# Kernel optimization log

Hardware: AMD Instinct MI355X
Metric: run time of the kernel (lower is better)

Reference implementation:

```python
import math
import jax, jax.numpy as jnp
import numpy as np

D_MODEL = 1024
D_CTX = 1024
NUM_HEADS = 16
ATTN_DIM = 1024
HEAD_DIM = ATTN_DIM // NUM_HEADS  # 64
ROPE_GAMMA = 10.0
ROTARY_BASE = 10000.0
ATTN_SCALE = math.sqrt(ATTN_DIM)  # note: module scales by sqrt(attn_dim), not sqrt(head_dim)


def _apply_rope(x, cos, sin):
    # x: [H,B,T,D]; cos/sin: [1,B,T,D//2]
    half = x.shape[-1] // 2
    x1, x2 = x[..., :half], x[..., half:]
    return jnp.concatenate([x1 * cos - x2 * sin, x1 * sin + x2 * cos], axis=-1)


def setup_inputs() -> dict:
    key = jax.random.key(0)
    ks = jax.random.split(key, 12)
    B, T, L = 4, 1024, 1024
    x = jax.random.normal(ks[0], (B, D_MODEL, T), jnp.float32)
    context = jax.random.normal(ks[1], (B, L, D_CTX), jnp.float32)
    # prefix (padding) masks with per-example valid lengths, as in real padded batches
    lens_q = jnp.array([1024, 896, 768, 640])
    lens_k = jnp.array([1024, 960, 832, 704])
    x_mask = (jnp.arange(T)[None, :] < lens_q[:, None]).astype(jnp.int32)[:, None, :]  # [B,1,T]
    context_mask = (jnp.arange(L)[None, :] < lens_k[:, None]).astype(jnp.int32)[:, None, :]  # [B,1,L]
    s = 0.02
    Wq = jax.random.normal(ks[2], (D_MODEL, ATTN_DIM), jnp.float32) * s
    bq = jax.random.normal(ks[3], (ATTN_DIM,), jnp.float32) * s
    Wk = jax.random.normal(ks[4], (D_CTX, ATTN_DIM), jnp.float32) * s
    bk = jax.random.normal(ks[5], (ATTN_DIM,), jnp.float32) * s
    Wv = jax.random.normal(ks[6], (D_CTX, ATTN_DIM), jnp.float32) * s
    bv = jax.random.normal(ks[7], (ATTN_DIM,), jnp.float32) * s
    Wo = jax.random.normal(ks[8], (ATTN_DIM, D_MODEL), jnp.float32) * s
    bo = jax.random.normal(ks[9], (D_MODEL,), jnp.float32) * s
    return {"x": x, "context": context, "x_mask": x_mask, "context_mask": context_mask,
            "Wq": Wq, "bq": bq, "Wk": Wk, "bk": bk, "Wv": Wv, "bv": bv, "Wo": Wo, "bo": bo}


def reference(x, context, x_mask, context_mask, Wq, bq, Wk, bk, Wv, bv, Wo, bo):
    B, _, T = x.shape
    L = context.shape[1]
    H, D = NUM_HEADS, HEAD_DIM
    xm = x_mask.astype(jnp.float32)          # [B,1,T]
    cmf = context_mask.astype(jnp.float32)   # [B,1,L]

    q = jnp.swapaxes(x, 1, 2) @ Wq + bq      # [B,T,attn_dim]
    k = context @ Wk + bk                    # [B,L,attn_dim]
    v = context @ Wv + bv                    # [B,L,attn_dim]

    q = q.reshape(B, T, H, D).transpose(2, 0, 1, 3)  # [H,B,T,D]
    k = k.reshape(B, L, H, D).transpose(2, 0, 1, 3)  # [H,B,L,D]
    v = v.reshape(B, L, H, D).transpose(2, 0, 1, 3)  # [H,B,L,D]

    # length-normalized RoPE (LARoPE)
    len_q = xm.sum(axis=(-2, -1)).reshape(-1, 1, 1)   # [B,1,1]
    len_k = cmf.sum(axis=(-2, -1)).reshape(-1, 1, 1)  # [B,1,1]
    pos_q = jnp.arange(T, dtype=jnp.float32).reshape(1, -1, 1)
    pos_k = jnp.arange(L, dtype=jnp.float32).reshape(1, -1, 1)
    inv_freq = 1.0 / (ROTARY_BASE ** (jnp.arange(0, D, 2, dtype=jnp.float32) / D))
    theta = (inv_freq * ROPE_GAMMA).reshape(1, 1, -1)  # [1,1,D//2]
    freqs_q = (pos_q / len_q) * theta  # [B,T,D//2]
    freqs_k = (pos_k / len_k) * theta  # [B,L,D//2]
    q = _apply_rope(q, jnp.cos(freqs_q)[None], jnp.sin(freqs_q)[None])
    k = _apply_rope(k, jnp.cos(freqs_k)[None], jnp.sin(freqs_k)[None])

    logits = jnp.einsum('hbtd,hbld->hbtl', q, k) / ATTN_SCALE  # [H,B,T,L]
    key_pad = (context_mask == 0)[None]  # [1,B,1,L]
    logits = jnp.where(key_pad, -jnp.inf, logits)
    attn = jax.nn.softmax(logits, axis=-1)
    query_pad = (x_mask == 0).transpose(1, 0, 2)[..., None]  # [1,B,T,1]
    attn = jnp.where(query_pad, 0.0, attn)

    out = jnp.einsum('hbtl,hbld->hbtd', attn, v)          # [H,B,T,D]
    out = out.transpose(1, 2, 0, 3).reshape(B, T, ATTN_DIM)
    out = out @ Wo + bo                                   # [B,T,d_model]
    out = out * jnp.swapaxes(xm, 1, 2)                    # [B,T,1] broadcast
    return jnp.swapaxes(out, 1, 2)                        # [B,d_model,T]
```

## Files before the change

kernel.cpp:

```cpp
#include <hip/hip_runtime.h>
#include <hip/hip_bf16.h>

typedef __attribute__((ext_vector_type(8))) short s8v;
typedef __attribute__((ext_vector_type(4))) float f4v;
typedef __attribute__((ext_vector_type(4))) unsigned short u4v;
typedef __attribute__((ext_vector_type(2))) unsigned int u2v;

#define NH 16

__device__ __forceinline__ unsigned short f2bf(float f) {
  union { float f; unsigned int u; } v; v.f = f;
  unsigned int r = (v.u + 0x7fffu + ((v.u >> 16) & 1u)) >> 16;
  return (unsigned short)r;
}
__device__ __forceinline__ void gll16(const void* g, void* l) {
  __builtin_amdgcn_global_load_lds((const __attribute__((address_space(1))) void*)g,
                                   (__attribute__((address_space(3))) void*)l, 16, 0, 0);
}
__device__ __forceinline__ unsigned int cvtpk(float lo, float hi) {
  unsigned int r;
  asm volatile("v_cvt_pk_bf16_f32 %0, %1, %2" : "=v"(r) : "v"(lo), "v"(hi));
  return r;
}

__global__ __launch_bounds__(256) void prep_kernel(
    const float* __restrict__ x, const float* __restrict__ ctx,
    const float* __restrict__ Wq, const float* __restrict__ Wk,
    const float* __restrict__ Wv, const float* __restrict__ Wo,
    const int* __restrict__ xm, const int* __restrict__ cm,
    unsigned short* __restrict__ xT, unsigned short* __restrict__ ctxb,
    unsigned short* __restrict__ WqT, unsigned short* __restrict__ WkT,
    unsigned short* __restrict__ WvT, unsigned short* __restrict__ WoT,
    float* __restrict__ lens) {
  const int z = blockIdx.z;
  const int tid = threadIdx.x;
  if (z == 12) {
    if (blockIdx.x | blockIdx.y) return;
    const int w = tid >> 6, lane = tid & 63;
    const int g = w * 2 + (lane >> 5);
    const int l32 = lane & 31;
    const int* m = (g < 4) ? (xm + g * 1024) : (cm + (g - 4) * 1024);
    int s = 0;
    for (int i = l32; i < 1024; i += 32) s += m[i];
    for (int o = 16; o; o >>= 1) s += __shfl_xor(s, o);
    if (l32 == 0) lens[g] = (float)s;
    return;
  }
  if (z >= 8) {
    const float* in = ctx + ((size_t)(z - 8) << 20);
    unsigned short* out = ctxb + ((size_t)(z - 8) << 20);
    const int i = (blockIdx.y * 32 + blockIdx.x) * 1024 + tid * 4;
    const f4v v = *(const f4v*)&in[i];
    u4v o;
#pragma unroll
    for (int j = 0; j < 4; ++j) o[j] = f2bf(v[j]);
    *(u4v*)&out[i] = o;
    return;
  }
  __shared__ unsigned short tile[32][33];
  const float* in;
  unsigned short* out;
  if (z < 4)      { in = x + ((size_t)z << 20); out = xT + ((size_t)z << 20); }
  else if (z == 4){ in = Wq; out = WqT; }
  else if (z == 5){ in = Wk; out = WkT; }
  else if (z == 6){ in = Wv; out = WvT; }
  else            { in = Wo; out = WoT; }
  const int r0 = blockIdx.y * 32, c0 = blockIdx.x * 32;
  const int tx = tid & 31, ty = tid >> 5;
  for (int i = ty; i < 32; i += 8) tile[i][tx] = f2bf(in[(size_t)(r0 + i) * 1024 + c0 + tx]);
  __syncthreads();
  for (int i = ty; i < 32; i += 8) out[(size_t)(c0 + i) * 1024 + r0 + tx] = tile[tx][i];
}

__global__ __launch_bounds__(256) void gemm_qkv_kernel(
    const unsigned short* __restrict__ xT, const unsigned short* __restrict__ ctxb,
    const unsigned short* __restrict__ WqT, const unsigned short* __restrict__ WkT,
    const unsigned short* __restrict__ WvT,
    const float* __restrict__ bq, const float* __restrict__ bk, const float* __restrict__ bv,
    unsigned short* __restrict__ Qb, unsigned short* __restrict__ Kb,
    unsigned short* __restrict__ Vtb, const float* __restrict__ lens) {
  __shared__ __attribute__((aligned(16))) unsigned short As[8192];
  __shared__ __attribute__((aligned(16))) unsigned short Bs[8192];
  const int mode = blockIdx.z;
  const unsigned short* A  = (mode == 0) ? xT : ctxb;
  const unsigned short* Bt = (mode == 0) ? WqT : (mode == 1) ? WkT : WvT;
  const float* bias        = (mode == 0) ? bq : (mode == 1) ? bk : bv;
  const int tid = threadIdx.x;
  const int lane = tid & 63, w = tid >> 6;
  const int lq = lane & 15, lg = lane >> 4;
  const int m0 = blockIdx.y * 128, n0 = blockIdx.x * 128;
  const int wm = (w & 1) * 64, wn = (w >> 1) * 64;
  const int cswz = (lq & 7) << 3;
  f4v acc[4][4] = {};

  for (int kt = 0; kt < 16; ++kt) {
    const int k0 = kt * 64;
#pragma unroll
    for (int i = 0; i < 4; ++i) {
      const int ci = i * 256 + tid;
      const int row = ci >> 3;
      const int col = ((ci & 7) * 8) ^ ((row & 7) << 3);
      gll16(&A[(size_t)(m0 + row) * 1024 + k0 + col], &As[ci * 8]);
      gll16(&Bt[(size_t)(n0 + row) * 1024 + k0 + col], &Bs[ci * 8]);
    }
    __syncthreads();
#pragma unroll
    for (int kc = 0; kc < 2; ++kc) {
      s8v af[4], bfr[4];
#pragma unroll
      for (int i = 0; i < 4; ++i)
        af[i] = *(const s8v*)&As[(wm + i * 16 + lq) * 64 + ((kc * 32 + lg * 8) ^ cswz)];
#pragma unroll
      for (int i = 0; i < 4; ++i)
        bfr[i] = *(const s8v*)&Bs[(wn + i * 16 + lq) * 64 + ((kc * 32 + lg * 8) ^ cswz)];
#pragma unroll
      for (int mi = 0; mi < 4; ++mi)
#pragma unroll
        for (int ni = 0; ni < 4; ++ni)
          acc[mi][ni] = __builtin_amdgcn_mfma_f32_16x16x32_bf16(af[mi], bfr[ni], acc[mi][ni], 0, 0, 0);
    }
    __syncthreads();
  }

  float bv4[4];
#pragma unroll
  for (int ni = 0; ni < 4; ++ni) bv4[ni] = bias[n0 + wn + ni * 16 + lq];
  const int b = m0 >> 10;

  if (mode <= 1) {
    unsigned short* O = mode ? Kb : Qb;
    const float len = lens[(mode ? 4 : 0) + b];
    const int h = (n0 + wn) >> 6;
#pragma unroll
    for (int mi = 0; mi < 4; ++mi) {
#pragma unroll
      for (int rr = 0; rr < 4; ++rr) {
        const int m = m0 + wm + mi * 16 + lg * 4 + rr;
        const int t = m & 1023;
        const float fb = (float)t / len * 10.0f;
#pragma unroll
        for (int ni = 0; ni < 2; ++ni) {
          const int jj = ni * 16 + lq;
          const float freq = fb * __expf((float)jj * -0.28782313662425572f);
          float sn, cs;
          __sincosf(freq, &sn, &cs);
          const float x1 = acc[mi][ni][rr] + bv4[ni];
          const float x2 = acc[mi][ni + 2][rr] + bv4[ni + 2];
          unsigned short* bp = &O[((size_t)((b * NH + h) * 1024 + t)) * 64 + jj];
          bp[0] = f2bf(x1 * cs - x2 * sn);
          bp[32] = f2bf(x1 * sn + x2 * cs);
        }
      }
    }
  } else {
#pragma unroll
    for (int mi = 0; mi < 4; ++mi) {
      const int mbase = m0 + wm + mi * 16 + lg * 4;
      const int l0 = mbase & 1023;
#pragma unroll
      for (int ni = 0; ni < 4; ++ni) {
        const int n = n0 + wn + ni * 16 + lq;
        const int hh = n >> 6, d = n & 63;
        u4v pk;
#pragma unroll
        for (int rr = 0; rr < 4; ++rr) pk[rr] = f2bf(acc[mi][ni][rr] + bv4[ni]);
        *(u4v*)&Vtb[((size_t)((b * NH + hh) * 64 + d)) * 1024 + l0] = pk;
      }
    }
  }
}

__global__ __launch_bounds__(256) void gemm_o_kernel(
    const unsigned short* __restrict__ A, const unsigned short* __restrict__ Bt,
    const float* __restrict__ bias, float* __restrict__ Cout,
    const int* __restrict__ xmask) {
  __shared__ __attribute__((aligned(16))) unsigned short As[8192];
  __shared__ __attribute__((aligned(16))) unsigned short Bs[8192];
  const int tid = threadIdx.x;
  const int lane = tid & 63, w = tid >> 6;
  const int lq = lane & 15, lg = lane >> 4;
  const int m0 = blockIdx.y * 128, n0 = blockIdx.x * 128;
  const int wm = (w & 1) * 64, wn = (w >> 1) * 64;
  const int cswz = (lq & 7) << 3;
  f4v acc[4][4] = {};

  for (int kt = 0; kt < 16; ++kt) {
    const int k0 = kt * 64;
#pragma unroll
    for (int i = 0; i < 4; ++i) {
      const int ci = i * 256 + tid;
      const int row = ci >> 3;
      const int col = ((ci & 7) * 8) ^ ((row & 7) << 3);
      gll16(&A[(size_t)(m0 + row) * 1024 + k0 + col], &As[ci * 8]);
      gll16(&Bt[(size_t)(n0 + row) * 1024 + k0 + col], &Bs[ci * 8]);
    }
    __syncthreads();
#pragma unroll
    for (int kc = 0; kc < 2; ++kc) {
      s8v af[4], bfr[4];
#pragma unroll
      for (int i = 0; i < 4; ++i)
        af[i] = *(const s8v*)&As[(wm + i * 16 + lq) * 64 + ((kc * 32 + lg * 8) ^ cswz)];
#pragma unroll
      for (int i = 0; i < 4; ++i)
        bfr[i] = *(const s8v*)&Bs[(wn + i * 16 + lq) * 64 + ((kc * 32 + lg * 8) ^ cswz)];
#pragma unroll
      for (int mi = 0; mi < 4; ++mi)
#pragma unroll
        for (int ni = 0; ni < 4; ++ni)
          acc[mi][ni] = __builtin_amdgcn_mfma_f32_16x16x32_bf16(af[mi], bfr[ni], acc[mi][ni], 0, 0, 0);
    }
    __syncthreads();
  }

  float bv4[4];
#pragma unroll
  for (int ni = 0; ni < 4; ++ni) bv4[ni] = bias[n0 + wn + ni * 16 + lq];
  const int b = m0 >> 10;
#pragma unroll
  for (int mi = 0; mi < 4; ++mi) {
    const int mbase = m0 + wm + mi * 16 + lg * 4;
    const int t0 = mbase & 1023;
#pragma unroll
    for (int ni = 0; ni < 4; ++ni) {
      const int n = n0 + wn + ni * 16 + lq;
      f4v pk;
#pragma unroll
      for (int rr = 0; rr < 4; ++rr) {
        float v = acc[mi][ni][rr] + bv4[ni];
        v *= (float)xmask[b * 1024 + t0 + rr];
        pk[rr] = v;
      }
      *(f4v*)&Cout[(size_t)b * 1024 * 1024 + (size_t)n * 1024 + t0] = pk;
    }
  }
}

__global__ __launch_bounds__(512) void attn_kernel(
    const unsigned short* __restrict__ Q, const unsigned short* __restrict__ K,
    const unsigned short* __restrict__ Vt, const float* __restrict__ lens,
    unsigned short* __restrict__ Aout) {
  __shared__ __attribute__((aligned(16))) unsigned short Ks[2][4096];
  __shared__ __attribute__((aligned(16))) unsigned short Vs[2][4096];
  __shared__ __attribute__((aligned(16))) unsigned short Plds[8][16][72];
  const int tid = threadIdx.x;
  const int lane = tid & 63, w = tid >> 6;
  const int lq = lane & 15, lg = lane >> 4;
  const int bh = blockIdx.y;
  const int b = bh >> 4, h = bh & 15;
  const int lenq = (int)lens[b];
  if ((int)blockIdx.x * 128 >= lenq) return;
  const int lenk = (int)lens[4 + b];
  const int nkt = (lenk + 63) >> 6;
  const int qrow = blockIdx.x * 128 + w * 16;
  const unsigned short* Qp = Q + ((size_t)bh * 1024 + qrow) * 64;
  const unsigned short* Kp = K + (size_t)bh * 65536;
  const unsigned short* Vp = Vt + (size_t)bh * 65536;
  const s8v qf0 = *(const s8v*)&Qp[lq * 64 + lg * 8];
  const s8v qf1 = *(const s8v*)&Qp[lq * 64 + 32 + lg * 8];
  const int r0 = tid >> 3;
  const int c0x = ((tid & 7) * 8) ^ ((r0 & 7) << 3);
  const int cswz = (lq & 7) << 3;

  gll16(&Kp[(size_t)r0 * 64 + c0x], &Ks[0][tid * 8]);
  gll16(&Vp[(size_t)r0 * 1024 + c0x], &Vs[0][tid * 8]);
  __syncthreads();

  const float SC2 = 0.0450842200277f;
  float m_run = -1e30f, s_run = 0.0f;
  f4v ot[4] = {};
  for (int kt = 0; kt < nkt; ++kt) {
    const int p = kt & 1;
    if (kt + 1 < nkt) {
      const int kn = (kt + 1) * 64;
      gll16(&Kp[(size_t)(kn + r0) * 64 + c0x], &Ks[p ^ 1][tid * 8]);
      gll16(&Vp[(size_t)r0 * 1024 + kn + c0x], &Vs[p ^ 1][tid * 8]);
    }
    const int k0 = kt * 64;
    const bool full = (k0 + 64 <= lenk);
    float pvv[16];
    float tmax = -1e30f;
    __builtin_amdgcn_s_setprio(1);
#pragma unroll
    for (int kk = 0; kk < 4; ++kk) {
      const int krow = kk * 16 + lq;
      const s8v a0 = *(const s8v*)&Ks[p][krow * 64 + ((lg * 8) ^ cswz)];
      const s8v a1 = *(const s8v*)&Ks[p][krow * 64 + ((32 + lg * 8) ^ cswz)];
      f4v s = {};
      s = __builtin_amdgcn_mfma_f32_16x16x32_bf16(a0, qf0, s, 0, 0, 0);
      s = __builtin_amdgcn_mfma_f32_16x16x32_bf16(a1, qf1, s, 0, 0, 0);
#pragma unroll
      for (int rr = 0; rr < 4; ++rr) {
        float v = s[rr] * SC2;
        if (!full) {
          const int key = k0 + kk * 16 + lg * 4 + rr;
          if (key >= lenk) v = -1e30f;
        }
        pvv[kk * 4 + rr] = v;
        tmax = fmaxf(tmax, v);
      }
    }
    __builtin_amdgcn_s_setprio(0);
    tmax = fmaxf(tmax, __shfl_xor(tmax, 16));
    tmax = fmaxf(tmax, __shfl_xor(tmax, 32));
    if (__any(tmax > m_run + 8.0f)) {
      const float m_new = fmaxf(m_run, tmax);
      const float alpha = exp2f(m_run - m_new);
#pragma unroll
      for (int d = 0; d < 4; ++d)
#pragma unroll
        for (int j = 0; j < 4; ++j) ot[d][j] *= alpha;
      s_run *= alpha;
      m_run = m_new;
    }
    float psum = 0.0f;
#pragma unroll
    for (int kk = 0; kk < 4; ++kk) {
      const float e0 = exp2f(pvv[kk * 4 + 0] - m_run);
      const float e1 = exp2f(pvv[kk * 4 + 1] - m_run);
      const float e2 = exp2f(pvv[kk * 4 + 2] - m_run);
      const float e3 = exp2f(pvv[kk * 4 + 3] - m_run);
      psum += (e0 + e1) + (e2 + e3);
      u2v pw;
      pw[0] = cvtpk(e0, e1);
      pw[1] = cvtpk(e2, e3);
      *(u2v*)&Plds[w][lq][kk * 16 + lg * 4] = pw;
    }
    psum += __shfl_xor(psum, 16);
    psum += __shfl_xor(psum, 32);
    s_run += psum;
    const s8v pb0 = *(const s8v*)&Plds[w][lq][lg * 8];
    const s8v pb1 = *(const s8v*)&Plds[w][lq][32 + lg * 8];
    __builtin_amdgcn_s_setprio(1);
#pragma unroll
    for (int d = 0; d < 4; ++d) {
      const int vrow = d * 16 + lq;
      const s8v av0 = *(const s8v*)&Vs[p][vrow * 64 + ((lg * 8) ^ cswz)];
      const s8v av1 = *(const s8v*)&Vs[p][vrow * 64 + ((32 + lg * 8) ^ cswz)];
      ot[d] = __builtin_amdgcn_mfma_f32_16x16x32_bf16(av0, pb0, ot[d], 0, 0, 0);
      ot[d] = __builtin_amdgcn_mfma_f32_16x16x32_bf16(av1, pb1, ot[d], 0, 0, 0);
    }
    __builtin_amdgcn_s_setprio(0);
    if (kt + 1 < nkt) __syncthreads();
  }
  const float inv = 1.0f / s_run;
  const int t = qrow + lq;
  unsigned short* op = Aout + ((size_t)(b * 1024 + t)) * 1024 + h * 64;
#pragma unroll
  for (int d = 0; d < 4; ++d) {
    u4v oo;
#pragma unroll
    for (int rr = 0; rr < 4; ++rr) oo[rr] = f2bf(ot[d][rr] * inv);
    *(u4v*)&op[d * 16 + lg * 4] = oo;
  }
}

extern "C" void kernel_launch(void* const* d_in, const int* in_sizes, int n_in,
                              void* d_out, int out_size, void* d_ws, size_t ws_size,
                              hipStream_t stream) {
  const float* x   = (const float*)d_in[0];
  const float* ctx = (const float*)d_in[1];
  const int* xm = (const int*)d_in[2];
  const int* cm = (const int*)d_in[3];
  const float* Wq = (const float*)d_in[4];
  const float* bq = (const float*)d_in[5];
  const float* Wk = (const float*)d_in[6];
  const float* bk = (const float*)d_in[7];
  const float* Wv = (const float*)d_in[8];
  const float* bv = (const float*)d_in[9];
  const float* Wo = (const float*)d_in[10];
  const float* bo = (const float*)d_in[11];

  char* ws = (char*)d_ws;
  const size_t MB = 1024 * 1024;
  unsigned short* xT   = (unsigned short*)(ws);
  unsigned short* AOb  = (unsigned short*)(ws);
  unsigned short* ctxb = (unsigned short*)(ws + 8 * MB);
  unsigned short* WqT  = (unsigned short*)(ws + 16 * MB);
  unsigned short* WkT  = (unsigned short*)(ws + 18 * MB);
  unsigned short* WvT  = (unsigned short*)(ws + 20 * MB);
  unsigned short* WoT  = (unsigned short*)(ws + 22 * MB);
  unsigned short* Qb   = (unsigned short*)(ws + 24 * MB);
  unsigned short* Kb   = (unsigned short*)(ws + 32 * MB);
  unsigned short* Vtb  = (unsigned short*)(ws + 40 * MB);
  float* lens          = (float*)(ws + 48 * MB);

  prep_kernel<<<dim3(32, 32, 13), 256, 0, stream>>>(x, ctx, Wq, Wk, Wv, Wo, xm, cm,
                                                    xT, ctxb, WqT, WkT, WvT, WoT, lens);
  gemm_qkv_kernel<<<dim3(8, 32, 3), 256, 0, stream>>>(xT, ctxb, WqT, WkT, WvT,
                                                      bq, bk, bv, Qb, Kb, Vtb, lens);
  attn_kernel<<<dim3(8, 64), 512, 0, stream>>>(Qb, Kb, Vtb, lens, AOb);
  gemm_o_kernel<<<dim3(8, 32), 256, 0, stream>>>(AOb, WoT, bo, (float*)d_out, xm);
}
```

Measured before the change: 125.4 us.

## Precompute RoPE cos/sin table in prep kernel and remap block indices

Adds a prep-kernel slice that recomputes mask lengths and writes a per-batch cos/sin table for Q and K positions, so the QKV GEMM epilogue loads float2 values instead of evaluating exp and sincos per element. It also remaps linear block IDs in the QKV GEMM, output GEMM and attention kernel so neighbouring blocks share M-rows or batch-heads, aiming at better L2 reuse. The cost is a 2 MB table write and read, plus extra blocks in prep, most of which exit immediately.

```diff
diff --git a/kernel.cpp b/kernel.cpp
--- a/kernel.cpp
+++ b/kernel.cpp
@@ -31,7 +31,7 @@
     unsigned short* __restrict__ xT, unsigned short* __restrict__ ctxb,
     unsigned short* __restrict__ WqT, unsigned short* __restrict__ WkT,
     unsigned short* __restrict__ WvT, unsigned short* __restrict__ WoT,
-    float* __restrict__ lens) {
+    float* __restrict__ lens, float2* __restrict__ rope) {
   const int z = blockIdx.z;
   const int tid = threadIdx.x;
   if (z == 12) {
@@ -46,6 +46,30 @@
     if (l32 == 0) lens[g] = (float)s;
     return;
   }
+  if (z == 13) {
+    const int idx = blockIdx.y * 32 + blockIdx.x;
+    if (idx >= 256) return;
+    const int which = idx >> 7;
+    const int b = (idx >> 5) & 3;
+    const int t0 = (idx & 31) * 32;
+    const int* m = (which ? cm : xm) + b * 1024;
+    const int lane = tid & 63;
+    int s = 0;
+    for (int i = lane; i < 1024; i += 64) s += m[i];
+    for (int o = 32; o; o >>= 1) s += __shfl_xor(s, o);
+    const float len = (float)s;
+    const int j = tid & 31;
+    const float theta = 10.0f * __expf((float)j * -0.28782313662425572f);
+    float2* rt = rope + ((size_t)(which * 4 + b) << 15);
+    for (int it = 0; it < 4; ++it) {
+      const int t = t0 + (tid >> 5) + it * 8;
+      const float fr = (float)t / len * theta;
+      float sn, cs;
+      __sincosf(fr, &sn, &cs);
+      rt[t * 32 + j] = make_float2(cs, sn);
+    }
+    return;
+  }
   if (z >= 8) {
     const float* in = ctx + ((size_t)(z - 8) << 20);
     unsigned short* out = ctxb + ((size_t)(z - 8) << 20);
@@ -78,17 +102,21 @@
     const unsigned short* __restrict__ WvT,
     const float* __restrict__ bq, const float* __restrict__ bk, const float* __restrict__ bv,
     unsigned short* __restrict__ Qb, unsigned short* __restrict__ Kb,
-    unsigned short* __restrict__ Vtb, const float* __restrict__ lens) {
+    unsigned short* __restrict__ Vtb, const float2* __restrict__ rope) {
   __shared__ __attribute__((aligned(16))) unsigned short As[8192];
   __shared__ __attribute__((aligned(16))) unsigned short Bs[8192];
-  const int mode = blockIdx.z;
+  const int id = blockIdx.x + (blockIdx.y << 3) + (blockIdx.z << 8);
+  const int rest = id >> 3;
+  const int my = (id & 7) + ((rest & 3) << 3);
+  const int nx = (rest >> 2) & 7;
+  const int mode = rest >> 5;
   const unsigned short* A  = (mode == 0) ? xT : ctxb;
   const unsigned short* Bt = (mode == 0) ? WqT : (mode == 1) ? WkT : WvT;
   const float* bias        = (mode == 0) ? bq : (mode == 1) ? bk : bv;
   const int tid = threadIdx.x;
   const int lane = tid & 63, w = tid >> 6;
   const int lq = lane & 15, lg = lane >> 4;
-  const int m0 = blockIdx.y * 128, n0 = blockIdx.x * 128;
+  const int m0 = my * 128, n0 = nx * 128;
   const int wm = (w & 1) * 64, wn = (w >> 1) * 64;
   const int cswz = (lq & 7) << 3;
   f4v acc[4][4] = {};
@@ -129,7 +157,7 @@
 
   if (mode <= 1) {
     unsigned short* O = mode ? Kb : Qb;
-    const float len = lens[(mode ? 4 : 0) + b];
+    const float2* rt = rope + ((size_t)(mode * 4 + b) << 15);
     const int h = (n0 + wn) >> 6;
 #pragma unroll
     for (int mi = 0; mi < 4; ++mi) {
@@ -137,18 +165,15 @@
       for (int rr = 0; rr < 4; ++rr) {
         const int m = m0 + wm + mi * 16 + lg * 4 + rr;
         const int t = m & 1023;
-        const float fb = (float)t / len * 10.0f;
 #pragma unroll
         for (int ni = 0; ni < 2; ++ni) {
           const int jj = ni * 16 + lq;
-          const float freq = fb * __expf((float)jj * -0.28782313662425572f);
-          float sn, cs;
-          __sincosf(freq, &sn, &cs);
+          const float2 cs2 = rt[t * 32 + jj];
           const float x1 = acc[mi][ni][rr] + bv4[ni];
           const float x2 = acc[mi][ni + 2][rr] + bv4[ni + 2];
           unsigned short* bp = &O[((size_t)((b * NH + h) * 1024 + t)) * 64 + jj];
-          bp[0] = f2bf(x1 * cs - x2 * sn);
-          bp[32] = f2bf(x1 * sn + x2 * cs);
+          bp[0] = f2bf(x1 * cs2.x - x2 * cs2.y);
+          bp[32] = f2bf(x1 * cs2.y + x2 * cs2.x);
         }
       }
     }
@@ -176,10 +201,14 @@
     const int* __restrict__ xmask) {
   __shared__ __attribute__((aligned(16))) unsigned short As[8192];
   __shared__ __attribute__((aligned(16))) unsigned short Bs[8192];
+  const int id = blockIdx.x + (blockIdx.y << 3);
+  const int rest = id >> 3;
+  const int my = (id & 7) + ((rest & 3) << 3);
+  const int nx = rest >> 2;
   const int tid = threadIdx.x;
   const int lane = tid & 63, w = tid >> 6;
   const int lq = lane & 15, lg = lane >> 4;
-  const int m0 = blockIdx.y * 128, n0 = blockIdx.x * 128;
+  const int m0 = my * 128, n0 = nx * 128;
   const int wm = (w & 1) * 64, wn = (w >> 1) * 64;
   const int cswz = (lq & 7) << 3;
   f4v acc[4][4] = {};
@@ -246,13 +275,15 @@
   const int tid = threadIdx.x;
   const int lane = tid & 63, w = tid >> 6;
   const int lq = lane & 15, lg = lane >> 4;
-  const int bh = blockIdx.y;
+  const int id = blockIdx.x + (blockIdx.y << 3);
+  const int bh = (id & 7) + (((id >> 3) & 7) << 3);
+  const int qblk = id >> 6;
   const int b = bh >> 4, h = bh & 15;
   const int lenq = (int)lens[b];
-  if ((int)blockIdx.x * 128 >= lenq) return;
+  if (qblk * 128 >= lenq) return;
   const int lenk = (int)lens[4 + b];
   const int nkt = (lenk + 63) >> 6;
-  const int qrow = blockIdx.x * 128 + w * 16;
+  const int qrow = qblk * 128 + w * 16;
   const unsigned short* Qp = Q + ((size_t)bh * 1024 + qrow) * 64;
   const unsigned short* Kp = K + (size_t)bh * 65536;
   const unsigned short* Vp = Vt + (size_t)bh * 65536;
@@ -384,11 +415,12 @@
   unsigned short* Kb   = (unsigned short*)(ws + 32 * MB);
   unsigned short* Vtb  = (unsigned short*)(ws + 40 * MB);
   float* lens          = (float*)(ws + 48 * MB);
-
-  prep_kernel<<<dim3(32, 32, 13), 256, 0, stream>>>(x, ctx, Wq, Wk, Wv, Wo, xm, cm,
-                                                    xT, ctxb, WqT, WkT, WvT, WoT, lens);
+  float2* rope         = (float2*)(ws + 49 * MB);
+
+  prep_kernel<<<dim3(32, 32, 14), 256, 0, stream>>>(x, ctx, Wq, Wk, Wv, Wo, xm, cm,
+                                                    xT, ctxb, WqT, WkT, WvT, WoT, lens, rope);
   gemm_qkv_kernel<<<dim3(8, 32, 3), 256, 0, stream>>>(xT, ctxb, WqT, WkT, WvT,
-                                                      bq, bk, bv, Qb, Kb, Vtb, lens);
+                                                      bq, bk, bv, Qb, Kb, Vtb, rope);
   attn_kernel<<<dim3(8, 64), 512, 0, stream>>>(Qb, Kb, Vtb, lens, AOb);
   gemm_o_kernel<<<dim3(8, 32), 256, 0, stream>>>(AOb, WoT, bo, (float*)d_out, xm);
 }
```

After: 123.9 us. No clear change (-1.2%).
